# Kernel tuning notes

Measured on AMD Instinct MI355X. Metric: run time of the kernel, lower is better.

The kernel has to match this reference:

```python
import jax, jax.numpy as jnp
import numpy as np

N_NODES = 50000
N_EDGES = 1600000
HID = 128
N_LAYERS = 3
N_GRAPHS = 64
LN_EPS = 1e-5


def setup_inputs() -> dict:
    key = jax.random.key(0)
    ks = jax.random.split(key, 8)
    x = jax.random.normal(ks[0], (N_NODES, HID), dtype=jnp.float32)
    edge_index = jax.random.randint(ks[1], (2, N_EDGES), 0, N_NODES)
    batch = jnp.sort(jax.random.randint(ks[2], (N_NODES,), 0, N_GRAPHS))
    s = 1.0 / np.sqrt(HID)
    Wn = jax.random.normal(ks[3], (N_LAYERS, HID, HID), dtype=jnp.float32) * s   # lin_l (neighbors)
    bn = jnp.zeros((N_LAYERS, HID), dtype=jnp.float32)                           # lin_l bias
    Wr = jax.random.normal(ks[4], (N_LAYERS, HID, HID), dtype=jnp.float32) * s   # lin_r (root), no bias
    gamma = jnp.ones((N_LAYERS, HID), dtype=jnp.float32)
    beta = jnp.zeros((N_LAYERS, HID), dtype=jnp.float32)
    return {"x": x, "Wn": Wn, "bn": bn, "Wr": Wr, "gamma": gamma, "beta": beta,
            "edge_index": edge_index, "batch": batch}


def _layer_norm(h, g, b):
    mu = jnp.mean(h, axis=-1, keepdims=True)
    var = jnp.mean((h - mu) ** 2, axis=-1, keepdims=True)
    return (h - mu) * jax.lax.rsqrt(var + LN_EPS) * g + b


def reference(x, Wn, bn, Wr, gamma, beta, edge_index, batch):
    src, dst = edge_index[0], edge_index[1]
    N = x.shape[0]
    # in-degree for mean aggregation (clamped to avoid div-by-zero for isolated nodes)
    deg = jax.ops.segment_sum(jnp.ones((src.shape[0],), x.dtype), dst, num_segments=N)
    inv_deg = 1.0 / jnp.maximum(deg, 1.0)
    for l in range(N_LAYERS):
        # SAGEConv: lin_l(mean_neighbor) + lin_r(x)
        agg = jax.ops.segment_sum(x[src], dst, num_segments=N) * inv_deg[:, None]
        h = agg @ Wn[l] + bn[l] + x @ Wr[l]
        h = _layer_norm(h, gamma[l], beta[l])
        x = jax.nn.relu(h)  # dropout is identity in eval mode
    node_emb = x
    cnt = jax.ops.segment_sum(jnp.ones((N,), x.dtype), batch, num_segments=N_GRAPHS)
    graph_emb = jax.ops.segment_sum(node_emb, batch, num_segments=N_GRAPHS) / jnp.maximum(cnt, 1.0)[:, None]
    return graph_emb, node_emb
```

## Files before the change

kernel.cpp:

```cpp
#include <hip/hip_runtime.h>

#define N_NODES 50000
#define N_EDGES 1600000
#define HID     128
#define N_GRAPHS 64

#define HB 256
#define EPB (N_EDGES / HB)
#define HWORDS 12500
#define NPP 12500
#define CWPP (NPP / 4)

#define WS_DEG   0u
#define WS_BSUM  50000u
#define WS_BOFF  50256u
#define WS_OFFS  50512u
#define WS_INVD  100512u
#define WS_CSR   150512u
#define WS_XB_B  1750512u
#define WS_XB_A  4950512u
#define WS_WP    8150512u
#define WS_END   8199664u

typedef __attribute__((ext_vector_type(8))) short short8;
typedef __attribute__((ext_vector_type(4))) float floatx4;

__device__ __forceinline__ float bf_lo(unsigned u) { return __uint_as_float(u << 16); }
__device__ __forceinline__ float bf_hi(unsigned u) { return __uint_as_float(u & 0xffff0000u); }
__device__ __forceinline__ unsigned bf_rn(float f) {
    unsigned u = __float_as_uint(f);
    unsigned r = ((u >> 16) & 1u) + 0x7fffu;
    return (u + r) >> 16;
}
__device__ __forceinline__ unsigned bf_pack(float lo, float hi) {
    return bf_rn(lo) | (bf_rn(hi) << 16);
}

__global__ __launch_bounds__(256) void k_prep(const float4* __restrict__ x, uint2* __restrict__ o,
                                              const float* __restrict__ Wn, const float* __restrict__ Wr,
                                              uint4* __restrict__ wp) {
    if (blockIdx.x < 6250) {
        int i = blockIdx.x * 256 + threadIdx.x;
        float4 v = x[i];
        uint2 r;
        r.x = bf_pack(v.x, v.y);
        r.y = bf_pack(v.z, v.w);
        o[i] = r;
    } else {
        int idx = (blockIdx.x - 6250) * 256 + threadIdx.x;
        int layer = idx >> 12;
        int rem = idx & 4095;
        int kb = rem >> 9;
        int n = (rem >> 2) & 127;
        int quad = rem & 3;
        float v[8];
#pragma unroll
        for (int j = 0; j < 8; j++) {
            int k = kb * 32 + quad * 8 + j;
            v[j] = (k < 128) ? Wn[layer * 16384 + k * 128 + n]
                             : Wr[layer * 16384 + (k - 128) * 128 + n];
        }
        uint4 r;
        r.x = bf_pack(v[0], v[1]);
        r.y = bf_pack(v[2], v[3]);
        r.z = bf_pack(v[4], v[5]);
        r.w = bf_pack(v[6], v[7]);
        wp[idx] = r;
    }
}


__global__ __launch_bounds__(256) void k_hist(const int* __restrict__ ei, unsigned* __restrict__ hist) {
    __shared__ unsigned sh[HWORDS];
    for (int i = threadIdx.x; i < HWORDS; i += 256) sh[i] = 0;
    __syncthreads();
    const int e0 = blockIdx.x * EPB;
    for (int i = threadIdx.x; i < EPB; i += 256) {
        int d = __builtin_nontemporal_load(ei + N_EDGES + e0 + i);
        atomicAdd(&sh[d >> 2], 1u << ((d & 3) << 3));
    }
    __syncthreads();
    unsigned* hb = hist + (size_t)blockIdx.x * HWORDS;
    for (int i = threadIdx.x; i < HWORDS; i += 256) hb[i] = sh[i];
}

__global__ __launch_bounds__(256) void k_scanb(unsigned* __restrict__ hist, int* __restrict__ deg,
                                               int* __restrict__ bsum) {
    int w = blockIdx.x * 256 + threadIdx.x;
    int mysum = 0;
    if (w < HWORDS) {
        unsigned run = 0;
#pragma unroll 8
        for (int b = 0; b < HB; ++b) {
            unsigned u = hist[(size_t)b * HWORDS + w];
            hist[(size_t)b * HWORDS + w] = run;
            run += u;
        }
#pragma unroll
        for (int k = 0; k < 4; ++k) {
            int d = (int)((run >> (k << 3)) & 0xffu);
            deg[4 * w + k] = d;
            mysum += d;
        }
    }
    __shared__ int s[256];
    s[threadIdx.x] = mysum;
    __syncthreads();
    for (int d = 128; d > 0; d >>= 1) {
        if (threadIdx.x < d) s[threadIdx.x] += s[threadIdx.x + d];
        __syncthreads();
    }
    if (threadIdx.x == 0) bsum[blockIdx.x] = s[0];
}

__global__ __launch_bounds__(256) void k_scanblocks(const int* __restrict__ bsum, int* __restrict__ boff, int nb) {
    __shared__ int s[256];
    int t = threadIdx.x;
    int v = (t < nb) ? bsum[t] : 0;
    s[t] = v;
    __syncthreads();
    for (int d = 1; d < 256; d <<= 1) {
        int add = (t >= d) ? s[t - d] : 0;
        __syncthreads();
        s[t] += add;
        __syncthreads();
    }
    if (t < nb) boff[t] = s[t] - v;
}

__global__ __launch_bounds__(256) void k_offsets(const int* __restrict__ deg, const int* __restrict__ boff,
                                                 int* __restrict__ offs, float* __restrict__ invdeg) {
    __shared__ int s[256];
    int b = blockIdx.x, t = threadIdx.x;
    int n0 = (b * 256 + t) * 4;
    int d[4] = {0, 0, 0, 0};
#pragma unroll
    for (int k = 0; k < 4; ++k)
        if (n0 + k < N_NODES) d[k] = deg[n0 + k];
    int v = d[0] + d[1] + d[2] + d[3];
    s[t] = v;
    __syncthreads();
    for (int dd = 1; dd < 256; dd <<= 1) {
        int add = (t >= dd) ? s[t - dd] : 0;
        __syncthreads();
        s[t] += add;
        __syncthreads();
    }
    int base = boff[b] + s[t] - v;
#pragma unroll
    for (int k = 0; k < 4; ++k) {
        if (n0 + k < N_NODES) {
            offs[n0 + k] = base;
            invdeg[n0 + k] = 1.0f / fmaxf((float)d[k], 1.0f);
            base += d[k];
        }
    }
}

__global__ __launch_bounds__(256) void k_fill(const int* __restrict__ ei, const int* __restrict__ offs,
                                              const unsigned* __restrict__ hist, int* __restrict__ csr) {
    __shared__ unsigned scur[CWPP];
    const int s8 = blockIdx.x & 7;
    const int pass = s8 >> 1;
    const int b = ((blockIdx.x >> 3) << 1) | (s8 & 1);
    const int nbase = pass * NPP;
    const unsigned* hb = hist + (size_t)b * HWORDS + pass * CWPP;
    for (int i = threadIdx.x; i < CWPP; i += 256) scur[i] = hb[i];
    __syncthreads();
    const int e0 = b * EPB;
    for (int i = threadIdx.x; i < EPB; i += 256) {
        int d = __builtin_nontemporal_load(ei + N_EDGES + e0 + i);
        unsigned rd = (unsigned)(d - nbase);
        if (rd < (unsigned)NPP) {
            int s = ei[e0 + i];
            int sh = (rd & 3) << 3;
            unsigned old = atomicAdd(&scur[rd >> 2], 1u << sh);
            unsigned rel = (old >> sh) & 0xffu;
            csr[offs[d] + (int)rel] = s * 16;
        }
    }
}


__global__ __launch_bounds__(256) void k_layer16(
        const uint4* __restrict__ xq, const int* __restrict__ csr,
        const int* __restrict__ offs, const int* __restrict__ deg,
        const float* __restrict__ invdeg, const uint4* __restrict__ wp,
        const float* __restrict__ bn, const float* __restrict__ gam,
        const float* __restrict__ bet, float* __restrict__ xout,
        unsigned* __restrict__ b16out, int write_f32) {
    __shared__ float H[16 * 132];
    uint4* A = (uint4*)H;

    const int t = threadIdx.x;
    const int wv = t >> 6;
    const int lane = t & 63;
    const int slot = lane >> 4;
    const int m = lane & 15;
    const int n0 = blockIdx.x * 16;
    const uint4* xm = xq + m;

    for (int i = 0; i < 4; ++i) {
        int node = __builtin_amdgcn_readfirstlane(n0 + wv * 4 + i);
        const int beg = offs[node];
        const int dn = deg[node];
        float a0 = 0.f, a1 = 0.f, a2 = 0.f, a3 = 0.f, a4 = 0.f, a5 = 0.f, a6 = 0.f, a7 = 0.f;
        int j = slot;
        for (; j + 32 <= dn; j += 32) {
            int s0 = csr[beg + j];
            int s1 = csr[beg + j + 4];
            int s2 = csr[beg + j + 8];
            int s3 = csr[beg + j + 12];
            int s4 = csr[beg + j + 16];
            int s5 = csr[beg + j + 20];
            int s6 = csr[beg + j + 24];
            int s7 = csr[beg + j + 28];
            uint4 u0 = xm[s0], u1 = xm[s1], u2 = xm[s2], u3 = xm[s3];
            uint4 u4 = xm[s4], u5 = xm[s5], u6 = xm[s6], u7 = xm[s7];
            a0 += ((bf_lo(u0.x) + bf_lo(u1.x)) + (bf_lo(u2.x) + bf_lo(u3.x))) + ((bf_lo(u4.x) + bf_lo(u5.x)) + (bf_lo(u6.x) + bf_lo(u7.x)));
            a1 += ((bf_hi(u0.x) + bf_hi(u1.x)) + (bf_hi(u2.x) + bf_hi(u3.x))) + ((bf_hi(u4.x) + bf_hi(u5.x)) + (bf_hi(u6.x) + bf_hi(u7.x)));
            a2 += ((bf_lo(u0.y) + bf_lo(u1.y)) + (bf_lo(u2.y) + bf_lo(u3.y))) + ((bf_lo(u4.y) + bf_lo(u5.y)) + (bf_lo(u6.y) + bf_lo(u7.y)));
            a3 += ((bf_hi(u0.y) + bf_hi(u1.y)) + (bf_hi(u2.y) + bf_hi(u3.y))) + ((bf_hi(u4.y) + bf_hi(u5.y)) + (bf_hi(u6.y) + bf_hi(u7.y)));
            a4 += ((bf_lo(u0.z) + bf_lo(u1.z)) + (bf_lo(u2.z) + bf_lo(u3.z))) + ((bf_lo(u4.z) + bf_lo(u5.z)) + (bf_lo(u6.z) + bf_lo(u7.z)));
            a5 += ((bf_hi(u0.z) + bf_hi(u1.z)) + (bf_hi(u2.z) + bf_hi(u3.z))) + ((bf_hi(u4.z) + bf_hi(u5.z)) + (bf_hi(u6.z) + bf_hi(u7.z)));
            a6 += ((bf_lo(u0.w) + bf_lo(u1.w)) + (bf_lo(u2.w) + bf_lo(u3.w))) + ((bf_lo(u4.w) + bf_lo(u5.w)) + (bf_lo(u6.w) + bf_lo(u7.w)));
            a7 += ((bf_hi(u0.w) + bf_hi(u1.w)) + (bf_hi(u2.w) + bf_hi(u3.w))) + ((bf_hi(u4.w) + bf_hi(u5.w)) + (bf_hi(u6.w) + bf_hi(u7.w)));
        }
        for (; j + 16 <= dn; j += 16) {
            int s0 = csr[beg + j];
            int s1 = csr[beg + j + 4];
            int s2 = csr[beg + j + 8];
            int s3 = csr[beg + j + 12];
            uint4 u0 = xm[s0], u1 = xm[s1], u2 = xm[s2], u3 = xm[s3];
            a0 += (bf_lo(u0.x) + bf_lo(u1.x)) + (bf_lo(u2.x) + bf_lo(u3.x));
            a1 += (bf_hi(u0.x) + bf_hi(u1.x)) + (bf_hi(u2.x) + bf_hi(u3.x));
            a2 += (bf_lo(u0.y) + bf_lo(u1.y)) + (bf_lo(u2.y) + bf_lo(u3.y));
            a3 += (bf_hi(u0.y) + bf_hi(u1.y)) + (bf_hi(u2.y) + bf_hi(u3.y));
            a4 += (bf_lo(u0.z) + bf_lo(u1.z)) + (bf_lo(u2.z) + bf_lo(u3.z));
            a5 += (bf_hi(u0.z) + bf_hi(u1.z)) + (bf_hi(u2.z) + bf_hi(u3.z));
            a6 += (bf_lo(u0.w) + bf_lo(u1.w)) + (bf_lo(u2.w) + bf_lo(u3.w));
            a7 += (bf_hi(u0.w) + bf_hi(u1.w)) + (bf_hi(u2.w) + bf_hi(u3.w));
        }
        for (; j < dn; j += 4) {
            uint4 u0 = xm[csr[beg + j]];
            a0 += bf_lo(u0.x); a1 += bf_hi(u0.x);
            a2 += bf_lo(u0.y); a3 += bf_hi(u0.y);
            a4 += bf_lo(u0.z); a5 += bf_hi(u0.z);
            a6 += bf_lo(u0.w); a7 += bf_hi(u0.w);
        }
#pragma unroll
        for (int msk = 16; msk < 64; msk <<= 1) {
            a0 += __shfl_xor(a0, msk); a1 += __shfl_xor(a1, msk);
            a2 += __shfl_xor(a2, msk); a3 += __shfl_xor(a3, msk);
            a4 += __shfl_xor(a4, msk); a5 += __shfl_xor(a5, msk);
            a6 += __shfl_xor(a6, msk); a7 += __shfl_xor(a7, msk);
        }
        if (slot == 0) {
            float id = invdeg[node];
            uint4 r;
            r.x = bf_pack(a0 * id, a1 * id);
            r.y = bf_pack(a2 * id, a3 * id);
            r.z = bf_pack(a4 * id, a5 * id);
            r.w = bf_pack(a6 * id, a7 * id);
            A[(wv * 4 + i) * 17 + m] = r;
        }
    }
    __syncthreads();

    const int quad = lane >> 4;
    const int nl = lane & 15;
    const int nb = wv * 32;
    floatx4 acc0 = {0.f, 0.f, 0.f, 0.f}, acc1 = acc0;
#pragma unroll
    for (int kb = 0; kb < 8; ++kb) {
        uint4 av = (kb < 4) ? A[nl * 17 + kb * 4 + quad]
                            : xq[(n0 + nl) * 16 + (kb - 4) * 4 + quad];
        uint4 b0 = wp[(kb * 128 + nb + nl) * 4 + quad];
        uint4 b1 = wp[(kb * 128 + nb + 16 + nl) * 4 + quad];
        short8 as = *(short8*)&av;
        short8 b0s = *(short8*)&b0, b1s = *(short8*)&b1;
        acc0 = __builtin_amdgcn_mfma_f32_16x16x32_bf16(as, b0s, acc0, 0, 0, 0);
        acc1 = __builtin_amdgcn_mfma_f32_16x16x32_bf16(as, b1s, acc1, 0, 0, 0);
    }
    __syncthreads();

    float bn0 = bn[nb + nl];
    float bn1 = bn[nb + 16 + nl];
#pragma unroll
    for (int reg = 0; reg < 4; ++reg) {
        int rr = quad * 4 + reg;
        H[rr * 132 + nb + nl] = acc0[reg] + bn0;
        H[rr * 132 + nb + 16 + nl] = acc1[reg] + bn1;
    }
    __syncthreads();

    const int row = t >> 4;
    const int sub = t & 15;
    const float* hr = &H[row * 132 + sub * 8];
    float v[8];
    float s = 0.f, s2 = 0.f;
#pragma unroll
    for (int i = 0; i < 8; i++) {
        v[i] = hr[i];
        s += v[i];
        s2 += v[i] * v[i];
    }
#pragma unroll
    for (int msk = 1; msk < 16; msk <<= 1) {
        s += __shfl_xor(s, msk);
        s2 += __shfl_xor(s2, msk);
    }
    float mean = s * (1.f / 128.f);
    float var = s2 * (1.f / 128.f) - mean * mean;
    float rstd = rsqrtf(var + 1e-5f);
    const int gr = n0 + row;
    const int cb = sub * 8;
    float o[8];
#pragma unroll
    for (int i = 0; i < 8; i++)
        o[i] = fmaxf((v[i] - mean) * rstd * gam[cb + i] + bet[cb + i], 0.f);
    if (write_f32) {
        *(float4*)&xout[(size_t)gr * HID + cb] = *(float4*)&o[0];
        *(float4*)&xout[(size_t)gr * HID + cb + 4] = *(float4*)&o[4];
    }
    unsigned p[4];
#pragma unroll
    for (int i = 0; i < 4; i++) p[i] = bf_pack(o[2 * i], o[2 * i + 1]);
    *(uint4*)&b16out[(size_t)gr * 64 + (cb >> 1)] = *(uint4*)&p[0];
}


__global__ __launch_bounds__(1024) void k_pool_seg(const unsigned* __restrict__ xb,
                                                   const int* __restrict__ batch,
                                                   float* __restrict__ out) {
    const int g = blockIdx.x;
    __shared__ int s_beg, s_end;
    if (threadIdx.x == 0) {
        int lo = 0, hi = N_NODES;
        while (lo < hi) { int mid = (lo + hi) >> 1; if (batch[mid] < g) lo = mid + 1; else hi = mid; }
        s_beg = lo;
        lo = 0; hi = N_NODES;
        while (lo < hi) { int mid = (lo + hi) >> 1; if (batch[mid] < g + 1) lo = mid + 1; else hi = mid; }
        s_end = lo;
    }
    __syncthreads();
    const int beg = s_beg, end = s_end;
    const int w = threadIdx.x & 63;
    const int q = threadIdx.x >> 6;
    float ax = 0.f, ay = 0.f;
    for (int r = beg + q; r < end; r += 16) {
        unsigned u = xb[(size_t)r * 64 + w];
        ax += bf_lo(u);
        ay += bf_hi(u);
    }
    __shared__ float sx[16][64], sy[16][64];
    sx[q][w] = ax;
    sy[q][w] = ay;
    __syncthreads();
    if (q == 0) {
        float tx = 0.f, ty = 0.f;
#pragma unroll
        for (int i = 0; i < 16; i++) { tx += sx[i][w]; ty += sy[i][w]; }
        float inv = 1.f / fmaxf((float)(end - beg), 1.f);
        float2 r;
        r.x = tx * inv;
        r.y = ty * inv;
        *(float2*)&out[(g << 7) + w * 2] = r;
    }
}

extern "C" void kernel_launch(void* const* d_in, const int* in_sizes, int n_in,
                              void* d_out, int out_size, void* d_ws, size_t ws_size,
                              hipStream_t stream) {
    const float* x0 = (const float*)d_in[0];
    const float* Wn = (const float*)d_in[1];
    const float* bn = (const float*)d_in[2];
    const float* Wr = (const float*)d_in[3];
    const float* gam = (const float*)d_in[4];
    const float* bet = (const float*)d_in[5];
    const int* ei = (const int*)d_in[6];
    const int* batch = (const int*)d_in[7];

    float* out = (float*)d_out;
    float* node_out = out + N_GRAPHS * HID;

    unsigned* ws = (unsigned*)d_ws;
    int* deg = (int*)(ws + WS_DEG);
    int* bsum = (int*)(ws + WS_BSUM);
    int* boff = (int*)(ws + WS_BOFF);
    int* offs = (int*)(ws + WS_OFFS);
    float* invdeg = (float*)(ws + WS_INVD);
    int* csr = (int*)(ws + WS_CSR);
    unsigned* hist = ws + WS_XB_B;
    unsigned* xa = ws + WS_XB_A;
    unsigned* xbb = ws + WS_XB_B;
    uint4* wp = (uint4*)(ws + WS_WP);

    k_prep<<<6298, 256, 0, stream>>>((const float4*)x0, (uint2*)xa, Wn, Wr, wp);
    k_hist<<<HB, 256, 0, stream>>>(ei, hist);
    k_scanb<<<49, 256, 0, stream>>>(hist, deg, bsum);
    k_scanblocks<<<1, 256, 0, stream>>>(bsum, boff, 49);
    k_offsets<<<49, 256, 0, stream>>>(deg, boff, offs, invdeg);
    k_fill<<<HB * 4, 256, 0, stream>>>(ei, offs, hist, csr);

    const int lb = N_NODES / 16;

    for (int l = 0; l < 3; ++l) {
        const unsigned* xin = (l & 1) ? xbb : xa;
        unsigned* xout16 = (l & 1) ? xa : xbb;
        k_layer16<<<lb, 256, 0, stream>>>((const uint4*)xin, csr, offs, deg, invdeg,
                                          wp + (size_t)l * 4096, bn + (size_t)l * HID,
                                          gam + (size_t)l * HID, bet + (size_t)l * HID,
                                          node_out, xout16, l == 2 ? 1 : 0);
    }

    k_pool_seg<<<N_GRAPHS, 1024, 0, stream>>>(xbb, batch, out);
}
```

Measured before the change: 464.8 us.

## Restructure CSR build with global-atomic histogram and two-level scan; split pooling

The per-block LDS histogram becomes one global atomic per edge into 200 slice histograms, which are zeroed by extra blocks in the prep kernel. The serial 256-deep column scan becomes a two-level scan over 8 groups, and the block-offset scan is folded into the offsets kernel, removing one launch. CSR index loads in the layer kernel become nontemporal. Graph pooling is split across four blocks per graph plus a small reduce kernel. The aim is more parallelism in the serial preprocessing stages and pooling, at the cost of many scattered global atomics and an extra zeroing pass over a large buffer.

```diff
diff --git a/kernel.cpp b/kernel.cpp
--- a/kernel.cpp
+++ b/kernel.cpp
@@ -5,11 +5,15 @@
 #define HID     128
 #define N_GRAPHS 64
 
-#define HB 256
+#define HB 200
 #define EPB (N_EDGES / HB)
 #define HWORDS 12500
 #define NPP 12500
 #define CWPP (NPP / 4)
+#define NGRP 8
+#define SPG (HB / NGRP)
+#define HZWORDS (HB * HWORDS)
+#define HZQ (HZWORDS / 4)
 
 #define WS_DEG   0u
 #define WS_BSUM  50000u
@@ -18,6 +22,7 @@
 #define WS_INVD  100512u
 #define WS_CSR   150512u
 #define WS_XB_B  1750512u
+#define WS_GSUM  (WS_XB_B + 2500000u)
 #define WS_XB_A  4950512u
 #define WS_WP    8150512u
 #define WS_END   8199664u
@@ -38,7 +43,7 @@
 
 __global__ __launch_bounds__(256) void k_prep(const float4* __restrict__ x, uint2* __restrict__ o,
                                               const float* __restrict__ Wn, const float* __restrict__ Wr,
-                                              uint4* __restrict__ wp) {
+                                              uint4* __restrict__ wp, uint4* __restrict__ hz) {
     if (blockIdx.x < 6250) {
         int i = blockIdx.x * 256 + threadIdx.x;
         float4 v = x[i];
@@ -46,7 +51,7 @@
         r.x = bf_pack(v.x, v.y);
         r.y = bf_pack(v.z, v.w);
         o[i] = r;
-    } else {
+    } else if (blockIdx.x < 6298) {
         int idx = (blockIdx.x - 6250) * 256 + threadIdx.x;
         int layer = idx >> 12;
         int rem = idx & 4095;
@@ -66,34 +71,49 @@
         r.z = bf_pack(v[4], v[5]);
         r.w = bf_pack(v[6], v[7]);
         wp[idx] = r;
+    } else {
+        int idx = (blockIdx.x - 6298) * 256 + threadIdx.x;
+        if (idx < HZQ) {
+            uint4 z = {0u, 0u, 0u, 0u};
+            hz[idx] = z;
+        }
     }
 }
 
 
 __global__ __launch_bounds__(256) void k_hist(const int* __restrict__ ei, unsigned* __restrict__ hist) {
-    __shared__ unsigned sh[HWORDS];
-    for (int i = threadIdx.x; i < HWORDS; i += 256) sh[i] = 0;
-    __syncthreads();
-    const int e0 = blockIdx.x * EPB;
-    for (int i = threadIdx.x; i < EPB; i += 256) {
-        int d = __builtin_nontemporal_load(ei + N_EDGES + e0 + i);
-        atomicAdd(&sh[d >> 2], 1u << ((d & 3) << 3));
-    }
-    __syncthreads();
-    unsigned* hb = hist + (size_t)blockIdx.x * HWORDS;
-    for (int i = threadIdx.x; i < HWORDS; i += 256) hb[i] = sh[i];
-}
-
-__global__ __launch_bounds__(256) void k_scanb(unsigned* __restrict__ hist, int* __restrict__ deg,
-                                               int* __restrict__ bsum) {
+    int e = blockIdx.x * 256 + threadIdx.x;
+    int d = __builtin_nontemporal_load(ei + N_EDGES + e);
+    int slice = e / EPB;
+    atomicAdd(&hist[(size_t)slice * HWORDS + (d >> 2)], 1u << ((d & 3) << 3));
+}
+
+__global__ __launch_bounds__(256) void k_scanb1(unsigned* __restrict__ hist, unsigned* __restrict__ gsum) {
+    int wb = blockIdx.x % 49;
+    int g = blockIdx.x / 49;
+    int w = wb * 256 + threadIdx.x;
+    if (w >= HWORDS) return;
+    size_t base = (size_t)(g * SPG) * HWORDS + w;
+    unsigned run = 0;
+#pragma unroll 5
+    for (int b = 0; b < SPG; ++b) {
+        unsigned u = hist[base + (size_t)b * HWORDS];
+        hist[base + (size_t)b * HWORDS] = run;
+        run += u;
+    }
+    gsum[(size_t)g * HWORDS + w] = run;
+}
+
+__global__ __launch_bounds__(256) void k_scanb2(unsigned* __restrict__ gsum, int* __restrict__ deg,
+                                                int* __restrict__ bsum) {
     int w = blockIdx.x * 256 + threadIdx.x;
     int mysum = 0;
     if (w < HWORDS) {
         unsigned run = 0;
-#pragma unroll 8
-        for (int b = 0; b < HB; ++b) {
-            unsigned u = hist[(size_t)b * HWORDS + w];
-            hist[(size_t)b * HWORDS + w] = run;
+#pragma unroll
+        for (int g = 0; g < NGRP; ++g) {
+            unsigned u = gsum[(size_t)g * HWORDS + w];
+            gsum[(size_t)g * HWORDS + w] = run;
             run += u;
         }
 #pragma unroll
@@ -113,31 +133,29 @@
     if (threadIdx.x == 0) bsum[blockIdx.x] = s[0];
 }
 
-__global__ __launch_bounds__(256) void k_scanblocks(const int* __restrict__ bsum, int* __restrict__ boff, int nb) {
-    __shared__ int s[256];
-    int t = threadIdx.x;
-    int v = (t < nb) ? bsum[t] : 0;
-    s[t] = v;
-    __syncthreads();
-    for (int d = 1; d < 256; d <<= 1) {
-        int add = (t >= d) ? s[t - d] : 0;
-        __syncthreads();
-        s[t] += add;
-        __syncthreads();
-    }
-    if (t < nb) boff[t] = s[t] - v;
-}
-
-__global__ __launch_bounds__(256) void k_offsets(const int* __restrict__ deg, const int* __restrict__ boff,
+__global__ __launch_bounds__(256) void k_offsets(const int* __restrict__ deg, const int* __restrict__ bsum,
                                                  int* __restrict__ offs, float* __restrict__ invdeg) {
+    __shared__ int sb[64], sb0[64];
     __shared__ int s[256];
     int b = blockIdx.x, t = threadIdx.x;
+    if (t < 64) {
+        int v = (t < 49) ? bsum[t] : 0;
+        sb[t] = v;
+        sb0[t] = v;
+    }
+    __syncthreads();
+    for (int d = 1; d < 64; d <<= 1) {
+        int add = (t < 64 && t >= d) ? sb[t - d] : 0;
+        __syncthreads();
+        if (t < 64) sb[t] += add;
+        __syncthreads();
+    }
     int n0 = (b * 256 + t) * 4;
-    int d[4] = {0, 0, 0, 0};
+    int dl[4] = {0, 0, 0, 0};
 #pragma unroll
     for (int k = 0; k < 4; ++k)
-        if (n0 + k < N_NODES) d[k] = deg[n0 + k];
-    int v = d[0] + d[1] + d[2] + d[3];
+        if (n0 + k < N_NODES) dl[k] = deg[n0 + k];
+    int v = dl[0] + dl[1] + dl[2] + dl[3];
     s[t] = v;
     __syncthreads();
     for (int dd = 1; dd < 256; dd <<= 1) {
@@ -146,26 +164,27 @@
         s[t] += add;
         __syncthreads();
     }
-    int base = boff[b] + s[t] - v;
+    int base = (sb[b] - sb0[b]) + s[t] - v;
 #pragma unroll
     for (int k = 0; k < 4; ++k) {
         if (n0 + k < N_NODES) {
             offs[n0 + k] = base;
-            invdeg[n0 + k] = 1.0f / fmaxf((float)d[k], 1.0f);
-            base += d[k];
+            invdeg[n0 + k] = 1.0f / fmaxf((float)dl[k], 1.0f);
+            base += dl[k];
         }
     }
 }
 
 __global__ __launch_bounds__(256) void k_fill(const int* __restrict__ ei, const int* __restrict__ offs,
-                                              const unsigned* __restrict__ hist, int* __restrict__ csr) {
+                                              const unsigned* __restrict__ hist,
+                                              const unsigned* __restrict__ gpre, int* __restrict__ csr) {
     __shared__ unsigned scur[CWPP];
-    const int s8 = blockIdx.x & 7;
-    const int pass = s8 >> 1;
-    const int b = ((blockIdx.x >> 3) << 1) | (s8 & 1);
+    const int pass = blockIdx.x & 3;
+    const int b = blockIdx.x >> 2;
     const int nbase = pass * NPP;
     const unsigned* hb = hist + (size_t)b * HWORDS + pass * CWPP;
-    for (int i = threadIdx.x; i < CWPP; i += 256) scur[i] = hb[i];
+    const unsigned* gb = gpre + (size_t)(b / SPG) * HWORDS + pass * CWPP;
+    for (int i = threadIdx.x; i < CWPP; i += 256) scur[i] = hb[i] + gb[i];
     __syncthreads();
     const int e0 = b * EPB;
     for (int i = threadIdx.x; i < EPB; i += 256) {
@@ -181,7 +200,6 @@
     }
 }
 
-
 __global__ __launch_bounds__(256) void k_layer16(
         const uint4* __restrict__ xq, const int* __restrict__ csr,
         const int* __restrict__ offs, const int* __restrict__ deg,
@@ -207,14 +225,14 @@
         float a0 = 0.f, a1 = 0.f, a2 = 0.f, a3 = 0.f, a4 = 0.f, a5 = 0.f, a6 = 0.f, a7 = 0.f;
         int j = slot;
         for (; j + 32 <= dn; j += 32) {
-            int s0 = csr[beg + j];
-            int s1 = csr[beg + j + 4];
-            int s2 = csr[beg + j + 8];
-            int s3 = csr[beg + j + 12];
-            int s4 = csr[beg + j + 16];
-            int s5 = csr[beg + j + 20];
-            int s6 = csr[beg + j + 24];
-            int s7 = csr[beg + j + 28];
+            int s0 = __builtin_nontemporal_load(csr + beg + j);
+            int s1 = __builtin_nontemporal_load(csr + beg + j + 4);
+            int s2 = __builtin_nontemporal_load(csr + beg + j + 8);
+            int s3 = __builtin_nontemporal_load(csr + beg + j + 12);
+            int s4 = __builtin_nontemporal_load(csr + beg + j + 16);
+            int s5 = __builtin_nontemporal_load(csr + beg + j + 20);
+            int s6 = __builtin_nontemporal_load(csr + beg + j + 24);
+            int s7 = __builtin_nontemporal_load(csr + beg + j + 28);
             uint4 u0 = xm[s0], u1 = xm[s1], u2 = xm[s2], u3 = xm[s3];
             uint4 u4 = xm[s4], u5 = xm[s5], u6 = xm[s6], u7 = xm[s7];
             a0 += ((bf_lo(u0.x) + bf_lo(u1.x)) + (bf_lo(u2.x) + bf_lo(u3.x))) + ((bf_lo(u4.x) + bf_lo(u5.x)) + (bf_lo(u6.x) + bf_lo(u7.x)));
@@ -227,10 +245,10 @@
             a7 += ((bf_hi(u0.w) + bf_hi(u1.w)) + (bf_hi(u2.w) + bf_hi(u3.w))) + ((bf_hi(u4.w) + bf_hi(u5.w)) + (bf_hi(u6.w) + bf_hi(u7.w)));
         }
         for (; j + 16 <= dn; j += 16) {
-            int s0 = csr[beg + j];
-            int s1 = csr[beg + j + 4];
-            int s2 = csr[beg + j + 8];
-            int s3 = csr[beg + j + 12];
+            int s0 = __builtin_nontemporal_load(csr + beg + j);
+            int s1 = __builtin_nontemporal_load(csr + beg + j + 4);
+            int s2 = __builtin_nontemporal_load(csr + beg + j + 8);
+            int s3 = __builtin_nontemporal_load(csr + beg + j + 12);
             uint4 u0 = xm[s0], u1 = xm[s1], u2 = xm[s2], u3 = xm[s3];
             a0 += (bf_lo(u0.x) + bf_lo(u1.x)) + (bf_lo(u2.x) + bf_lo(u3.x));
             a1 += (bf_hi(u0.x) + bf_hi(u1.x)) + (bf_hi(u2.x) + bf_hi(u3.x));
@@ -242,7 +260,7 @@
             a7 += (bf_hi(u0.w) + bf_hi(u1.w)) + (bf_hi(u2.w) + bf_hi(u3.w));
         }
         for (; j < dn; j += 4) {
-            uint4 u0 = xm[csr[beg + j]];
+            uint4 u0 = xm[__builtin_nontemporal_load(csr + beg + j)];
             a0 += bf_lo(u0.x); a1 += bf_hi(u0.x);
             a2 += bf_lo(u0.y); a3 += bf_hi(u0.y);
             a4 += bf_lo(u0.z); a5 += bf_hi(u0.z);
@@ -330,10 +348,12 @@
 }
 
 
-__global__ __launch_bounds__(1024) void k_pool_seg(const unsigned* __restrict__ xb,
-                                                   const int* __restrict__ batch,
-                                                   float* __restrict__ out) {
-    const int g = blockIdx.x;
+__global__ __launch_bounds__(1024) void k_pool1(const unsigned* __restrict__ xb,
+                                                const int* __restrict__ batch,
+                                                float* __restrict__ partial, int* __restrict__ cnt) {
+    const int bid = blockIdx.x;
+    const int g = bid >> 2;
+    const int part = bid & 3;
     __shared__ int s_beg, s_end;
     if (threadIdx.x == 0) {
         int lo = 0, hi = N_NODES;
@@ -348,8 +368,8 @@
     const int w = threadIdx.x & 63;
     const int q = threadIdx.x >> 6;
     float ax = 0.f, ay = 0.f;
-    for (int r = beg + q; r < end; r += 16) {
-        unsigned u = xb[(size_t)r * 64 + w];
+    for (int r = beg + part * 16 + q; r < end; r += 64) {
+        unsigned u = __builtin_nontemporal_load(xb + (size_t)r * 64 + w);
         ax += bf_lo(u);
         ay += bf_hi(u);
     }
@@ -361,12 +381,24 @@
         float tx = 0.f, ty = 0.f;
 #pragma unroll
         for (int i = 0; i < 16; i++) { tx += sx[i][w]; ty += sy[i][w]; }
-        float inv = 1.f / fmaxf((float)(end - beg), 1.f);
         float2 r;
-        r.x = tx * inv;
-        r.y = ty * inv;
-        *(float2*)&out[(g << 7) + w * 2] = r;
-    }
+        r.x = tx;
+        r.y = ty;
+        *(float2*)&partial[(size_t)bid * 128 + w * 2] = r;
+    }
+    if (part == 0 && threadIdx.x == 0) cnt[g] = end - beg;
+}
+
+__global__ __launch_bounds__(256) void k_pool2(const float* __restrict__ partial,
+                                               const int* __restrict__ cnt,
+                                               float* __restrict__ out) {
+    int idx = blockIdx.x * 256 + threadIdx.x;
+    int g = idx >> 7;
+    float s = partial[(size_t)(g * 4 + 0) * 128 + (idx & 127)]
+            + partial[(size_t)(g * 4 + 1) * 128 + (idx & 127)]
+            + partial[(size_t)(g * 4 + 2) * 128 + (idx & 127)]
+            + partial[(size_t)(g * 4 + 3) * 128 + (idx & 127)];
+    out[idx] = s / fmaxf((float)cnt[g], 1.f);
 }
 
 extern "C" void kernel_launch(void* const* d_in, const int* in_sizes, int n_in,
@@ -387,21 +419,23 @@
     unsigned* ws = (unsigned*)d_ws;
     int* deg = (int*)(ws + WS_DEG);
     int* bsum = (int*)(ws + WS_BSUM);
-    int* boff = (int*)(ws + WS_BOFF);
     int* offs = (int*)(ws + WS_OFFS);
     float* invdeg = (float*)(ws + WS_INVD);
     int* csr = (int*)(ws + WS_CSR);
     unsigned* hist = ws + WS_XB_B;
+    unsigned* gsum = ws + WS_GSUM;
     unsigned* xa = ws + WS_XB_A;
     unsigned* xbb = ws + WS_XB_B;
     uint4* wp = (uint4*)(ws + WS_WP);
-
-    k_prep<<<6298, 256, 0, stream>>>((const float4*)x0, (uint2*)xa, Wn, Wr, wp);
-    k_hist<<<HB, 256, 0, stream>>>(ei, hist);
-    k_scanb<<<49, 256, 0, stream>>>(hist, deg, bsum);
-    k_scanblocks<<<1, 256, 0, stream>>>(bsum, boff, 49);
-    k_offsets<<<49, 256, 0, stream>>>(deg, boff, offs, invdeg);
-    k_fill<<<HB * 4, 256, 0, stream>>>(ei, offs, hist, csr);
+    float* partial = (float*)(ws + WS_CSR);
+    int* cnt = (int*)(ws + WS_CSR + 256 * 128);
+
+    k_prep<<<8740, 256, 0, stream>>>((const float4*)x0, (uint2*)xa, Wn, Wr, wp, (uint4*)hist);
+    k_hist<<<6250, 256, 0, stream>>>(ei, hist);
+    k_scanb1<<<NGRP * 49, 256, 0, stream>>>(hist, gsum);
+    k_scanb2<<<49, 256, 0, stream>>>(gsum, deg, bsum);
+    k_offsets<<<49, 256, 0, stream>>>(deg, bsum, offs, invdeg);
+    k_fill<<<HB * 4, 256, 0, stream>>>(ei, offs, hist, gsum, csr);
 
     const int lb = N_NODES / 16;
 
@@ -414,5 +448,6 @@
                                           node_out, xout16, l == 2 ? 1 : 0);
     }
 
-    k_pool_seg<<<N_GRAPHS, 1024, 0, stream>>>(xbb, batch, out);
-}
+    k_pool1<<<N_GRAPHS * 4, 1024, 0, stream>>>(xbb, batch, partial, cnt);
+    k_pool2<<<32, 256, 0, stream>>>(partial, cnt, out);
+}
```

Result: slower. 524.8 us (+12.9%).
